# Kernel optimization log

Measured on AMD Instinct MI355X. Metric: run time of the kernel, lower is better.

## Reference

```python
import jax, jax.numpy as jnp
import numpy as np

B, N, D, H = 4, 1024, 1024, 16
NP = N - 1  # prototypes; +1 CLS slot -> n_valid == N
HD = D // H
LN_EPS = 1e-5


def _build_spatial_sim(key):
    centers = jax.random.uniform(key, (NP, 2), dtype=jnp.float32) * 10.0
    diff = centers[:, None, :] - centers[None, :, :]
    d2 = jnp.sum(diff * diff, axis=-1)           # squared pairwise distance
    dist = jnp.sqrt(d2)
    sigma = dist.mean()                           # spatial_sigma = mean cdist
    sim = jnp.exp(-d2 / (2.0 * sigma * sigma))
    sim = sim / sim.max()
    ext = jnp.zeros((NP + 1, NP + 1), dtype=jnp.float32)
    ext = ext.at[0, :].set(1.0).at[:, 0].set(1.0).at[1:, 1:].set(sim)
    return ext


def setup_inputs() -> dict:
    key = jax.random.key(0)
    kc, kx, kq, kp = jax.random.split(key, 4)
    spatial_sim = _build_spatial_sim(kc)          # [N, N] buffer
    x = jax.random.normal(kx, (B, N, D), dtype=jnp.float32)
    gamma = jnp.ones((D,), dtype=jnp.float32)
    beta = jnp.zeros((D,), dtype=jnp.float32)
    w_qkv = jax.random.normal(kq, (D, 3 * D), dtype=jnp.float32) * 0.02
    w_proj = jax.random.normal(kp, (D, D), dtype=jnp.float32) * 0.02
    b_proj = jnp.zeros((D,), dtype=jnp.float32)
    swl = jnp.float32(np.log(0.3 / 0.7))          # inverse_sigmoid(0.3)
    return {"x": x, "gamma": gamma, "beta": beta, "w_qkv": w_qkv,
            "w_proj": w_proj, "b_proj": b_proj,
            "spatial_weight_logit": swl, "spatial_sim": spatial_sim}


def reference(x, gamma, beta, w_qkv, w_proj, b_proj, spatial_weight_logit, spatial_sim):
    b, n, d = x.shape
    scale = HD ** (-0.5)
    # LayerNorm (biased variance, eps=1e-5)
    mu = x.mean(axis=-1, keepdims=True)
    var = jnp.mean((x - mu) ** 2, axis=-1, keepdims=True)
    x_norm = (x - mu) / jnp.sqrt(var + LN_EPS) * gamma + beta
    # QKV projection -> [B, H, N, HD] each
    qkv = (x_norm @ w_qkv).reshape(b, n, 3, H, HD)
    qkv = jnp.transpose(qkv, (2, 0, 3, 1, 4))
    q, k, v = qkv[0], qkv[1], qkv[2]
    scores = jnp.einsum('bhnd,bhmd->bhnm', q, k) * scale
    alpha = jax.nn.sigmoid(spatial_weight_logit)
    # blend feature attention with fixed spatial similarity, then softmax
    attn = jax.nn.softmax((1.0 - alpha) * scores + alpha * spatial_sim[None, None], axis=-1)
    out = jnp.einsum('bhnm,bhmd->bhnd', attn, v)
    out = jnp.transpose(out, (0, 2, 1, 3)).reshape(b, n, d)
    out = out @ w_proj + b_proj
    return x + out
```

## Files before the change

### kernel.cpp

```cpp
#include <hip/hip_runtime.h>

#define Bz 4
#define Nn 1024
#define Dd 1024
#define Hh 16
#define HD 64
#define SCALE 0.125f
#define LN_EPS 1e-5f

typedef __attribute__((ext_vector_type(8))) __bf16 bf16x8;
typedef __attribute__((ext_vector_type(4))) float f32x4;

static __device__ inline unsigned short f2bf(float f) {
    unsigned int u = __float_as_uint(f);
    u += 0x7fffu + ((u >> 16) & 1u);
    return (unsigned short)(u >> 16);
}

static __device__ inline bf16x8 ldfrag(const unsigned short* p) {
    return *(const bf16x8*)p;
}

static __device__ __forceinline__ void glds16(const unsigned short* g, unsigned short* l) {
    __builtin_amdgcn_global_load_lds((const __attribute__((address_space(1))) void*)g,
                                     (__attribute__((address_space(3))) void*)l, 16, 0, 0);
}

__global__ __launch_bounds__(256) void prep_kernel(const float* __restrict__ x,
                                                   const float* __restrict__ gamma,
                                                   const float* __restrict__ beta,
                                                   unsigned short* __restrict__ xn,
                                                   const float* __restrict__ w_qkv,
                                                   unsigned short* __restrict__ wqkvT,
                                                   const float* __restrict__ w_proj,
                                                   unsigned short* __restrict__ wprojT) {
    __shared__ float tile[32][33];
    int blk = blockIdx.x;
    int tid = threadIdx.x;

    if (blk < 4096) {
        const float* xr = x + (size_t)blk * Dd;
        float4 v = ((const float4*)xr)[tid];
        float s = v.x + v.y + v.z + v.w;
        float ss = v.x * v.x + v.y * v.y + v.z * v.z + v.w * v.w;
        for (int o = 32; o > 0; o >>= 1) {
            s += __shfl_down(s, o);
            ss += __shfl_down(ss, o);
        }
        float* red = &tile[0][0];
        int wid = tid >> 6;
        if ((tid & 63) == 0) { red[wid * 2] = s; red[wid * 2 + 1] = ss; }
        __syncthreads();
        float tot = red[0] + red[2] + red[4] + red[6];
        float tot2 = red[1] + red[3] + red[5] + red[7];
        float mu = tot * (1.0f / Dd);
        float var = tot2 * (1.0f / Dd) - mu * mu;
        float inv = rsqrtf(var + LN_EPS);
        float4 g = ((const float4*)gamma)[tid];
        float4 b = ((const float4*)beta)[tid];
        ushort4 o4;
        o4.x = f2bf((v.x - mu) * inv * g.x + b.x);
        o4.y = f2bf((v.y - mu) * inv * g.y + b.y);
        o4.z = f2bf((v.z - mu) * inv * g.z + b.z);
        o4.w = f2bf((v.w - mu) * inv * g.w + b.w);
        ((ushort4*)(xn + (size_t)blk * Dd))[tid] = o4;
    } else {
        const float* in;
        unsigned short* out;
        int cols, c0, r0;
        if (blk < 7168) {
            int idx = blk - 4096;
            in = w_qkv; out = wqkvT; cols = 3072;
            c0 = (idx % 96) * 32; r0 = (idx / 96) * 32;
        } else {
            int idx = blk - 7168;
            in = w_proj; out = wprojT; cols = 1024;
            c0 = (idx % 32) * 32; r0 = (idx / 32) * 32;
        }
        int tx = tid & 31, ty = tid >> 5;
        #pragma unroll
        for (int i = 0; i < 32; i += 8)
            tile[ty + i][tx] = in[(size_t)(r0 + ty + i) * cols + c0 + tx];
        __syncthreads();
        #pragma unroll
        for (int i = 0; i < 32; i += 8)
            out[(size_t)(c0 + ty + i) * 1024 + r0 + tx] = f2bf(tile[tx][ty + i]);
    }
}


__global__ __launch_bounds__(256) void gemm_qkv(const unsigned short* __restrict__ A,
                                                const unsigned short* __restrict__ Bt,
                                                unsigned short* __restrict__ qb,
                                                unsigned short* __restrict__ kb,
                                                unsigned short* __restrict__ vtb) {
    __shared__ unsigned short sA[8192], sB[8192];
    int tid = threadIdx.x;
    int w = tid >> 6, lane = tid & 63, lrow = lane & 15, quad = lane >> 4;
    int wm = w >> 1, wn = w & 1;
    int rowbase = blockIdx.y * 128;
    int colbase = blockIdx.x * 128;

    int srow = tid >> 3;
    int gch = ((tid & 7) - (srow >> 1)) & 7;
    const unsigned short* gA = A + (size_t)(rowbase + srow) * 1024 + gch * 8;
    const unsigned short* gB = Bt + (size_t)(colbase + srow) * 1024 + gch * 8;
    unsigned short* lA = sA + w * 512;
    unsigned short* lB = sB + w * 512;

    int bs0 = ((quad + (lrow >> 1)) & 7) * 8;
    int bs1 = ((4 + quad + (lrow >> 1)) & 7) * 8;
    const unsigned short* fa = sA + (wm * 64 + lrow) * 64;
    const unsigned short* fb = sB + (wn * 64 + lrow) * 64;

    f32x4 acc[4][4];
    #pragma unroll
    for (int i = 0; i < 4; i++)
        #pragma unroll
        for (int j = 0; j < 4; j++)
            acc[i][j] = (f32x4){0.f, 0.f, 0.f, 0.f};

    for (int k0 = 0; k0 < 1024; k0 += 64) {
        __syncthreads();
        #pragma unroll
        for (int c = 0; c < 4; c++) {
            glds16(gA + (size_t)c * 32768 + k0, lA + c * 2048);
            glds16(gB + (size_t)c * 32768 + k0, lB + c * 2048);
        }
        __syncthreads();
        #pragma unroll
        for (int s = 0; s < 2; s++) {
            int bo = s ? bs1 : bs0;
            bf16x8 a[4], b[4];
            #pragma unroll
            for (int i = 0; i < 4; i++) a[i] = *(const bf16x8*)(fa + i * 1024 + bo);
            #pragma unroll
            for (int j = 0; j < 4; j++) b[j] = *(const bf16x8*)(fb + j * 1024 + bo);
            #pragma unroll
            for (int i = 0; i < 4; i++)
                #pragma unroll
                for (int j = 0; j < 4; j++)
                    acc[i][j] = __builtin_amdgcn_mfma_f32_16x16x32_bf16(a[i], b[j], acc[i][j], 0, 0, 0);
        }
    }

    if (colbase < 2048) {
        #pragma unroll
        for (int j = 0; j < 4; j++) {
            int col = colbase + wn * 64 + j * 16 + lrow;
            int s = col >> 10, rem = col & 1023;
            int h = rem >> 6, e = rem & 63;
            unsigned short* dst = (s == 0) ? qb : kb;
            #pragma unroll
            for (int i = 0; i < 4; i++) {
                #pragma unroll
                for (int r = 0; r < 4; r++) {
                    int R = rowbase + wm * 64 + i * 16 + quad * 4 + r;
                    int bb = R >> 10, n = R & 1023;
                    dst[(((size_t)(bb * Hh + h)) * Nn + n) * HD + e] = f2bf(acc[i][j][r]);
                }
            }
        }
    } else {
        int bb = rowbase >> 10;
        int nbase = (rowbase & 1023) + wm * 64;
        unsigned short* sc = sA + w * 2048;
        int er = lane >> 2, nc = lane & 3;
        #pragma unroll
        for (int j = 0; j < 4; j++) {
            __syncthreads();
            int ebase = colbase + wn * 64 + j * 16 - 2048;
            int h = ebase >> 6, e0 = ebase & 63;
            #pragma unroll
            for (int i = 0; i < 4; i++) {
                uint2 pk;
                pk.x = (unsigned)f2bf(acc[i][j][0]) | ((unsigned)f2bf(acc[i][j][1]) << 16);
                pk.y = (unsigned)f2bf(acc[i][j][2]) | ((unsigned)f2bf(acc[i][j][3]) << 16);
                *(uint2*)(sc + lrow * 68 + i * 16 + quad * 4) = pk;
            }
            __syncthreads();
            unsigned short* vrow = vtb + ((size_t)((bb * Hh + h) * HD) + e0 + er) * Nn + nbase;
            #pragma unroll
            for (int c = 0; c < 4; c++) {
                uint2 v = *(const uint2*)(sc + er * 68 + c * 16 + nc * 4);
                *(uint2*)(vrow + c * 16 + nc * 4) = v;
            }
        }
    }
}

__global__ __launch_bounds__(256) void gemm_proj(const unsigned short* __restrict__ A,
                                                 const unsigned short* __restrict__ Bt,
                                                 const float* __restrict__ bias,
                                                 const float* __restrict__ x,
                                                 float* __restrict__ out) {
    __shared__ unsigned short sA[8192], sB[8192];
    int tid = threadIdx.x;
    int w = tid >> 6, lane = tid & 63, lrow = lane & 15, quad = lane >> 4;
    int wm = w >> 1, wn = w & 1;
    int rowbase = blockIdx.y * 128;
    int colbase = blockIdx.x * 128;

    int srow = tid >> 3;
    int gch = ((tid & 7) - (srow >> 1)) & 7;
    const unsigned short* gA = A + (size_t)(rowbase + srow) * 1024 + gch * 8;
    const unsigned short* gB = Bt + (size_t)(colbase + srow) * 1024 + gch * 8;
    unsigned short* lA = sA + w * 512;
    unsigned short* lB = sB + w * 512;

    int bs0 = ((quad + (lrow >> 1)) & 7) * 8;
    int bs1 = ((4 + quad + (lrow >> 1)) & 7) * 8;
    const unsigned short* fa = sA + (wm * 64 + lrow) * 64;
    const unsigned short* fb = sB + (wn * 64 + lrow) * 64;

    f32x4 acc[4][4];
    #pragma unroll
    for (int i = 0; i < 4; i++)
        #pragma unroll
        for (int j = 0; j < 4; j++)
            acc[i][j] = (f32x4){0.f, 0.f, 0.f, 0.f};

    for (int k0 = 0; k0 < 1024; k0 += 64) {
        __syncthreads();
        #pragma unroll
        for (int c = 0; c < 4; c++) {
            glds16(gA + (size_t)c * 32768 + k0, lA + c * 2048);
            glds16(gB + (size_t)c * 32768 + k0, lB + c * 2048);
        }
        __syncthreads();
        #pragma unroll
        for (int s = 0; s < 2; s++) {
            int bo = s ? bs1 : bs0;
            bf16x8 a[4], b[4];
            #pragma unroll
            for (int i = 0; i < 4; i++) a[i] = *(const bf16x8*)(fa + i * 1024 + bo);
            #pragma unroll
            for (int j = 0; j < 4; j++) b[j] = *(const bf16x8*)(fb + j * 1024 + bo);
            #pragma unroll
            for (int i = 0; i < 4; i++)
                #pragma unroll
                for (int j = 0; j < 4; j++)
                    acc[i][j] = __builtin_amdgcn_mfma_f32_16x16x32_bf16(a[i], b[j], acc[i][j], 0, 0, 0);
        }
    }

    #pragma unroll
    for (int j = 0; j < 4; j++) {
        int col = colbase + wn * 64 + j * 16 + lrow;
        float bc = bias[col];
        #pragma unroll
        for (int i = 0; i < 4; i++) {
            #pragma unroll
            for (int r = 0; r < 4; r++) {
                int R = rowbase + wm * 64 + i * 16 + quad * 4 + r;
                out[(size_t)R * 1024 + col] = acc[i][j][r] + bc + x[(size_t)R * 1024 + col];
            }
        }
    }
}

#define PSTR 72
__global__ __launch_bounds__(256) void attn_kernel(const unsigned short* __restrict__ qb,
                                                   const unsigned short* __restrict__ kb,
                                                   const unsigned short* __restrict__ vtb,
                                                   const float* __restrict__ sim,
                                                   const float* __restrict__ swl,
                                                   unsigned short* __restrict__ aout) {
    int h = blockIdx.y, bb = blockIdx.z;
    int n0 = blockIdx.x * 128;
    int tid = threadIdx.x;
    int w = tid >> 6, lane = tid & 63;
    int lrow = lane & 15, quad = lane >> 4;
    const unsigned short* q = qb + ((size_t)(bb * Hh + h)) * Nn * HD;
    const unsigned short* k = kb + ((size_t)(bb * Hh + h)) * Nn * HD;
    const unsigned short* vt = vtb + ((size_t)(bb * Hh + h)) * HD * Nn;
    float alpha = 1.f / (1.f + __expf(-swl[0]));
    float c1 = (1.f - alpha) * SCALE;

    __shared__ unsigned short sK[4096];
    __shared__ unsigned short sV[4096];
    __shared__ unsigned short sP[128 * PSTR];

    int qr0 = n0 + w * 32;
    bf16x8 qf[2][2];
    #pragma unroll
    for (int g = 0; g < 2; g++) {
        qf[g][0] = ldfrag(q + (size_t)(qr0 + g * 16 + lrow) * HD + quad * 8);
        qf[g][1] = ldfrag(q + (size_t)(qr0 + g * 16 + lrow) * HD + 32 + quad * 8);
    }

    f32x4 o[2][4];
    #pragma unroll
    for (int g = 0; g < 2; g++)
        #pragma unroll
        for (int et = 0; et < 4; et++) o[g][et] = (f32x4){0.f, 0.f, 0.f, 0.f};
    float rsum[2] = {0.f, 0.f};

    int bs0 = (quad + (lrow >> 1)) & 7;
    int bs1 = (4 + quad + (lrow >> 1)) & 7;
    unsigned short* sPw = sP + (w * 32) * PSTR;

    for (int m0 = 0; m0 < 1024; m0 += 64) {
        __syncthreads();
        #pragma unroll
        for (int i = 0; i < 2; i++) {
            int slot = i * 256 + tid;
            int row = slot >> 3;
            int cg = ((slot & 7) - (row >> 1)) & 7;
            glds16(k + (size_t)(m0 + row) * HD + cg * 8, sK + i * 2048 + w * 512);
        }
        #pragma unroll
        for (int i = 0; i < 2; i++) {
            int slot = i * 256 + tid;
            int row = slot >> 3;
            int cg = ((slot & 7) - (row >> 1)) & 7;
            glds16(vt + (size_t)row * Nn + m0 + cg * 8, sV + i * 2048 + w * 512);
        }
        float4 sm[4][2];
        #pragma unroll
        for (int ks = 0; ks < 4; ks++)
            #pragma unroll
            for (int g = 0; g < 2; g++)
                sm[ks][g] = *(const float4*)(sim + (size_t)(qr0 + g * 16 + lrow) * Nn
                                             + m0 + ks * 16 + quad * 4);
        __syncthreads();

        #pragma unroll
        for (int ks = 0; ks < 4; ks++) {
            const unsigned short* kr = sK + (ks * 16 + lrow) * 64;
            bf16x8 ak0 = *(const bf16x8*)(kr + bs0 * 8);
            bf16x8 ak1 = *(const bf16x8*)(kr + bs1 * 8);
            #pragma unroll
            for (int g = 0; g < 2; g++) {
                f32x4 c = (f32x4){0.f, 0.f, 0.f, 0.f};
                c = __builtin_amdgcn_mfma_f32_16x16x32_bf16(ak0, qf[g][0], c, 0, 0, 0);
                c = __builtin_amdgcn_mfma_f32_16x16x32_bf16(ak1, qf[g][1], c, 0, 0, 0);
                float e0 = __expf(c1 * c[0] + alpha * sm[ks][g].x);
                float e1 = __expf(c1 * c[1] + alpha * sm[ks][g].y);
                float e2 = __expf(c1 * c[2] + alpha * sm[ks][g].z);
                float e3 = __expf(c1 * c[3] + alpha * sm[ks][g].w);
                rsum[g] += (e0 + e1) + (e2 + e3);
                uint2 pk;
                pk.x = (__float_as_uint(e0) >> 16) | (__float_as_uint(e1) & 0xffff0000u);
                pk.y = (__float_as_uint(e2) >> 16) | (__float_as_uint(e3) & 0xffff0000u);
                *(uint2*)(sPw + (g * 16 + lrow) * PSTR + ks * 16 + quad * 4) = pk;
            }
        }

        #pragma unroll
        for (int ms = 0; ms < 2; ms++) {
            bf16x8 pa[2];
            #pragma unroll
            for (int g = 0; g < 2; g++)
                pa[g] = *(const bf16x8*)(sPw + (g * 16 + lrow) * PSTR + ms * 32 + quad * 8);
            #pragma unroll
            for (int et = 0; et < 4; et++) {
                int e = et * 16 + lrow;
                int slot = (ms * 4 + quad + (e >> 1)) & 7;
                bf16x8 vb = *(const bf16x8*)(sV + e * 64 + slot * 8);
                #pragma unroll
                for (int g = 0; g < 2; g++)
                    o[g][et] = __builtin_amdgcn_mfma_f32_16x16x32_bf16(pa[g], vb, o[g][et], 0, 0, 0);
            }
        }
    }

    #pragma unroll
    for (int g = 0; g < 2; g++) {
        rsum[g] += __shfl_xor(rsum[g], 16);
        rsum[g] += __shfl_xor(rsum[g], 32);
    }

    #pragma unroll
    for (int g = 0; g < 2; g++)
        #pragma unroll
        for (int r = 0; r < 4; r++) {
            float inv = 1.f / __shfl(rsum[g], quad * 4 + r);
            int qn = qr0 + g * 16 + quad * 4 + r;
            #pragma unroll
            for (int et = 0; et < 4; et++)
                aout[((size_t)bb * Nn + qn) * Dd + h * HD + et * 16 + lrow]
                    = f2bf(o[g][et][r] * inv);
        }
}

extern "C" void kernel_launch(void* const* d_in, const int* in_sizes, int n_in,
                              void* d_out, int out_size, void* d_ws, size_t ws_size,
                              hipStream_t stream) {
    const float* x      = (const float*)d_in[0];
    const float* gamma  = (const float*)d_in[1];
    const float* beta   = (const float*)d_in[2];
    const float* w_qkv  = (const float*)d_in[3];
    const float* w_proj = (const float*)d_in[4];
    const float* b_proj = (const float*)d_in[5];
    const float* swl    = (const float*)d_in[6];
    const float* sim    = (const float*)d_in[7];
    float* out = (float*)d_out;

    unsigned short* ws = (unsigned short*)d_ws;
    unsigned short* xn     = ws;
    unsigned short* wqkvT  = xn + 4194304;
    unsigned short* wprojT = wqkvT + 3145728;
    unsigned short* qb     = wprojT + 1048576;
    unsigned short* kb     = qb + 4194304;
    unsigned short* vtb    = kb + 4194304;
    unsigned short* aout   = vtb + 4194304;

    prep_kernel<<<8192, 256, 0, stream>>>(x, gamma, beta, xn, w_qkv, wqkvT, w_proj, wprojT);
    gemm_qkv<<<dim3(24, 32), 256, 0, stream>>>(xn, wqkvT, qb, kb, vtb);
    attn_kernel<<<dim3(8, 16, 4), 256, 0, stream>>>(qb, kb, vtb, sim, swl, aout);
    gemm_proj<<<dim3(8, 32), 256, 0, stream>>>(aout, wprojT, b_proj, x, out);
}
```

Before: 199.4 us.

## Fuse all stages into one cooperative persistent kernel with grid syncs

```diff
diff --git a/kernel.cpp b/kernel.cpp
--- a/kernel.cpp
+++ b/kernel.cpp
@@ -1,4 +1,7 @@
 #include <hip/hip_runtime.h>
+#include <hip/hip_cooperative_groups.h>
+
+namespace cg = cooperative_groups;
 
 #define Bz 4
 #define Nn 1024
@@ -26,80 +29,74 @@
                                      (__attribute__((address_space(3))) void*)l, 16, 0, 0);
 }
 
-__global__ __launch_bounds__(256) void prep_kernel(const float* __restrict__ x,
-                                                   const float* __restrict__ gamma,
-                                                   const float* __restrict__ beta,
-                                                   unsigned short* __restrict__ xn,
-                                                   const float* __restrict__ w_qkv,
-                                                   unsigned short* __restrict__ wqkvT,
-                                                   const float* __restrict__ w_proj,
-                                                   unsigned short* __restrict__ wprojT) {
-    __shared__ float tile[32][33];
-    int blk = blockIdx.x;
-    int tid = threadIdx.x;
-
-    if (blk < 4096) {
-        const float* xr = x + (size_t)blk * Dd;
-        float4 v = ((const float4*)xr)[tid];
-        float s = v.x + v.y + v.z + v.w;
-        float ss = v.x * v.x + v.y * v.y + v.z * v.z + v.w * v.w;
-        for (int o = 32; o > 0; o >>= 1) {
-            s += __shfl_down(s, o);
-            ss += __shfl_down(ss, o);
-        }
-        float* red = &tile[0][0];
-        int wid = tid >> 6;
-        if ((tid & 63) == 0) { red[wid * 2] = s; red[wid * 2 + 1] = ss; }
-        __syncthreads();
-        float tot = red[0] + red[2] + red[4] + red[6];
-        float tot2 = red[1] + red[3] + red[5] + red[7];
-        float mu = tot * (1.0f / Dd);
-        float var = tot2 * (1.0f / Dd) - mu * mu;
-        float inv = rsqrtf(var + LN_EPS);
-        float4 g = ((const float4*)gamma)[tid];
-        float4 b = ((const float4*)beta)[tid];
-        ushort4 o4;
-        o4.x = f2bf((v.x - mu) * inv * g.x + b.x);
-        o4.y = f2bf((v.y - mu) * inv * g.y + b.y);
-        o4.z = f2bf((v.z - mu) * inv * g.z + b.z);
-        o4.w = f2bf((v.w - mu) * inv * g.w + b.w);
-        ((ushort4*)(xn + (size_t)blk * Dd))[tid] = o4;
-    } else {
-        const float* in;
-        unsigned short* out;
-        int cols, c0, r0;
-        if (blk < 7168) {
-            int idx = blk - 4096;
-            in = w_qkv; out = wqkvT; cols = 3072;
-            c0 = (idx % 96) * 32; r0 = (idx / 96) * 32;
+static __device__ __forceinline__ void phase_prep(unsigned short* smem, int bid, int tid,
+        const float* __restrict__ x, const float* __restrict__ gamma,
+        const float* __restrict__ beta, unsigned short* __restrict__ xn,
+        const float* __restrict__ w_qkv, unsigned short* __restrict__ wqkvT,
+        const float* __restrict__ w_proj, unsigned short* __restrict__ wprojT) {
+    float* tile = (float*)smem;
+    for (int blk = bid; blk < 8192; blk += 512) {
+        if (blk < 4096) {
+            const float* xr = x + (size_t)blk * Dd;
+            float4 v = ((const float4*)xr)[tid];
+            float s = v.x + v.y + v.z + v.w;
+            float ss = v.x * v.x + v.y * v.y + v.z * v.z + v.w * v.w;
+            for (int o = 32; o > 0; o >>= 1) {
+                s += __shfl_down(s, o);
+                ss += __shfl_down(ss, o);
+            }
+            int wid = tid >> 6;
+            if ((tid & 63) == 0) { tile[wid * 2] = s; tile[wid * 2 + 1] = ss; }
+            __syncthreads();
+            float tot = tile[0] + tile[2] + tile[4] + tile[6];
+            float tot2 = tile[1] + tile[3] + tile[5] + tile[7];
+            float mu = tot * (1.0f / Dd);
+            float var = tot2 * (1.0f / Dd) - mu * mu;
+            float inv = rsqrtf(var + LN_EPS);
+            float4 g = ((const float4*)gamma)[tid];
+            float4 b = ((const float4*)beta)[tid];
+            ushort4 o4;
+            o4.x = f2bf((v.x - mu) * inv * g.x + b.x);
+            o4.y = f2bf((v.y - mu) * inv * g.y + b.y);
+            o4.z = f2bf((v.z - mu) * inv * g.z + b.z);
+            o4.w = f2bf((v.w - mu) * inv * g.w + b.w);
+            ((ushort4*)(xn + (size_t)blk * Dd))[tid] = o4;
         } else {
-            int idx = blk - 7168;
-            in = w_proj; out = wprojT; cols = 1024;
-            c0 = (idx % 32) * 32; r0 = (idx / 32) * 32;
-        }
-        int tx = tid & 31, ty = tid >> 5;
-        #pragma unroll
-        for (int i = 0; i < 32; i += 8)
-            tile[ty + i][tx] = in[(size_t)(r0 + ty + i) * cols + c0 + tx];
-        __syncthreads();
-        #pragma unroll
-        for (int i = 0; i < 32; i += 8)
-            out[(size_t)(c0 + ty + i) * 1024 + r0 + tx] = f2bf(tile[tx][ty + i]);
-    }
-}
-
-
-__global__ __launch_bounds__(256) void gemm_qkv(const unsigned short* __restrict__ A,
-                                                const unsigned short* __restrict__ Bt,
-                                                unsigned short* __restrict__ qb,
-                                                unsigned short* __restrict__ kb,
-                                                unsigned short* __restrict__ vtb) {
-    __shared__ unsigned short sA[8192], sB[8192];
-    int tid = threadIdx.x;
+            const float* in;
+            unsigned short* outp;
+            int cols, c0, r0;
+            if (blk < 7168) {
+                int idx = blk - 4096;
+                in = w_qkv; outp = wqkvT; cols = 3072;
+                c0 = (idx % 96) * 32; r0 = (idx / 96) * 32;
+            } else {
+                int idx = blk - 7168;
+                in = w_proj; outp = wprojT; cols = 1024;
+                c0 = (idx % 32) * 32; r0 = (idx / 32) * 32;
+            }
+            int tx = tid & 31, ty = tid >> 5;
+            #pragma unroll
+            for (int i = 0; i < 32; i += 8)
+                tile[(ty + i) * 33 + tx] = in[(size_t)(r0 + ty + i) * cols + c0 + tx];
+            __syncthreads();
+            #pragma unroll
+            for (int i = 0; i < 32; i += 8)
+                outp[(size_t)(c0 + ty + i) * 1024 + r0 + tx] = f2bf(tile[tx * 33 + ty + i]);
+        }
+        __syncthreads();
+    }
+}
+
+static __device__ __forceinline__ void phase_qkv(unsigned short* smem, int t, int tid,
+        const unsigned short* __restrict__ A, const unsigned short* __restrict__ Bt,
+        unsigned short* __restrict__ qb, unsigned short* __restrict__ kb,
+        unsigned short* __restrict__ vtb) {
+    unsigned short* sA = smem;
+    unsigned short* sB = smem + 8192;
     int w = tid >> 6, lane = tid & 63, lrow = lane & 15, quad = lane >> 4;
     int wm = w >> 1, wn = w & 1;
-    int rowbase = blockIdx.y * 128;
-    int colbase = blockIdx.x * 128;
+    int rowbase = (t >> 5) * 128;
+    int colbase = (t & 31) * 96;
 
     int srow = tid >> 3;
     int gch = ((tid & 7) - (srow >> 1)) & 7;
@@ -111,45 +108,47 @@
     int bs0 = ((quad + (lrow >> 1)) & 7) * 8;
     int bs1 = ((4 + quad + (lrow >> 1)) & 7) * 8;
     const unsigned short* fa = sA + (wm * 64 + lrow) * 64;
-    const unsigned short* fb = sB + (wn * 64 + lrow) * 64;
-
-    f32x4 acc[4][4];
+    const unsigned short* fb = sB + (wn * 48 + lrow) * 64;
+
+    f32x4 acc[4][3];
     #pragma unroll
     for (int i = 0; i < 4; i++)
         #pragma unroll
-        for (int j = 0; j < 4; j++)
+        for (int j = 0; j < 3; j++)
             acc[i][j] = (f32x4){0.f, 0.f, 0.f, 0.f};
 
     for (int k0 = 0; k0 < 1024; k0 += 64) {
         __syncthreads();
         #pragma unroll
-        for (int c = 0; c < 4; c++) {
+        for (int c = 0; c < 4; c++)
             glds16(gA + (size_t)c * 32768 + k0, lA + c * 2048);
+        #pragma unroll
+        for (int c = 0; c < 3; c++)
             glds16(gB + (size_t)c * 32768 + k0, lB + c * 2048);
-        }
         __syncthreads();
         #pragma unroll
         for (int s = 0; s < 2; s++) {
             int bo = s ? bs1 : bs0;
-            bf16x8 a[4], b[4];
+            bf16x8 a[4], b[3];
             #pragma unroll
             for (int i = 0; i < 4; i++) a[i] = *(const bf16x8*)(fa + i * 1024 + bo);
             #pragma unroll
-            for (int j = 0; j < 4; j++) b[j] = *(const bf16x8*)(fb + j * 1024 + bo);
+            for (int j = 0; j < 3; j++) b[j] = *(const bf16x8*)(fb + j * 1024 + bo);
             #pragma unroll
             for (int i = 0; i < 4; i++)
                 #pragma unroll
-                for (int j = 0; j < 4; j++)
+                for (int j = 0; j < 3; j++)
                     acc[i][j] = __builtin_amdgcn_mfma_f32_16x16x32_bf16(a[i], b[j], acc[i][j], 0, 0, 0);
         }
     }
 
-    if (colbase < 2048) {
-        #pragma unroll
-        for (int j = 0; j < 4; j++) {
-            int col = colbase + wn * 64 + j * 16 + lrow;
-            int s = col >> 10, rem = col & 1023;
-            int h = rem >> 6, e = rem & 63;
+    #pragma unroll
+    for (int j = 0; j < 3; j++) {
+        int colg = colbase + wn * 48 + j * 16;
+        int s = colg >> 10, rem = colg & 1023;
+        int h = rem >> 6;
+        int e = (rem & 63) + lrow;
+        if (s < 2) {
             unsigned short* dst = (s == 0) ? qb : kb;
             #pragma unroll
             for (int i = 0; i < 4; i++) {
@@ -160,126 +159,38 @@
                     dst[(((size_t)(bb * Hh + h)) * Nn + n) * HD + e] = f2bf(acc[i][j][r]);
                 }
             }
-        }
-    } else {
-        int bb = rowbase >> 10;
-        int nbase = (rowbase & 1023) + wm * 64;
-        unsigned short* sc = sA + w * 2048;
-        int er = lane >> 2, nc = lane & 3;
-        #pragma unroll
-        for (int j = 0; j < 4; j++) {
-            __syncthreads();
-            int ebase = colbase + wn * 64 + j * 16 - 2048;
-            int h = ebase >> 6, e0 = ebase & 63;
+        } else {
             #pragma unroll
             for (int i = 0; i < 4; i++) {
+                int R0 = rowbase + wm * 64 + i * 16 + quad * 4;
+                int bb = R0 >> 10, n0v = R0 & 1023;
                 uint2 pk;
                 pk.x = (unsigned)f2bf(acc[i][j][0]) | ((unsigned)f2bf(acc[i][j][1]) << 16);
                 pk.y = (unsigned)f2bf(acc[i][j][2]) | ((unsigned)f2bf(acc[i][j][3]) << 16);
-                *(uint2*)(sc + lrow * 68 + i * 16 + quad * 4) = pk;
-            }
-            __syncthreads();
-            unsigned short* vrow = vtb + ((size_t)((bb * Hh + h) * HD) + e0 + er) * Nn + nbase;
-            #pragma unroll
-            for (int c = 0; c < 4; c++) {
-                uint2 v = *(const uint2*)(sc + er * 68 + c * 16 + nc * 4);
-                *(uint2*)(vrow + c * 16 + nc * 4) = v;
-            }
-        }
-    }
-}
-
-__global__ __launch_bounds__(256) void gemm_proj(const unsigned short* __restrict__ A,
-                                                 const unsigned short* __restrict__ Bt,
-                                                 const float* __restrict__ bias,
-                                                 const float* __restrict__ x,
-                                                 float* __restrict__ out) {
-    __shared__ unsigned short sA[8192], sB[8192];
-    int tid = threadIdx.x;
+                *(uint2*)(vtb + ((size_t)((bb * Hh + h) * HD) + e) * Nn + n0v) = pk;
+            }
+        }
+    }
+}
+
+static __device__ __forceinline__ void phase_attn(unsigned short* smem, int bid, int tid,
+        const unsigned short* __restrict__ qb, const unsigned short* __restrict__ kb,
+        const unsigned short* __restrict__ vtb, const float* __restrict__ sim,
+        const float* __restrict__ swl, unsigned short* __restrict__ aout) {
+    int nt = bid & 7, h = (bid >> 3) & 15, bb = bid >> 7;
+    int n0 = nt * 128;
     int w = tid >> 6, lane = tid & 63, lrow = lane & 15, quad = lane >> 4;
-    int wm = w >> 1, wn = w & 1;
-    int rowbase = blockIdx.y * 128;
-    int colbase = blockIdx.x * 128;
-
-    int srow = tid >> 3;
-    int gch = ((tid & 7) - (srow >> 1)) & 7;
-    const unsigned short* gA = A + (size_t)(rowbase + srow) * 1024 + gch * 8;
-    const unsigned short* gB = Bt + (size_t)(colbase + srow) * 1024 + gch * 8;
-    unsigned short* lA = sA + w * 512;
-    unsigned short* lB = sB + w * 512;
-
-    int bs0 = ((quad + (lrow >> 1)) & 7) * 8;
-    int bs1 = ((4 + quad + (lrow >> 1)) & 7) * 8;
-    const unsigned short* fa = sA + (wm * 64 + lrow) * 64;
-    const unsigned short* fb = sB + (wn * 64 + lrow) * 64;
-
-    f32x4 acc[4][4];
-    #pragma unroll
-    for (int i = 0; i < 4; i++)
-        #pragma unroll
-        for (int j = 0; j < 4; j++)
-            acc[i][j] = (f32x4){0.f, 0.f, 0.f, 0.f};
-
-    for (int k0 = 0; k0 < 1024; k0 += 64) {
-        __syncthreads();
-        #pragma unroll
-        for (int c = 0; c < 4; c++) {
-            glds16(gA + (size_t)c * 32768 + k0, lA + c * 2048);
-            glds16(gB + (size_t)c * 32768 + k0, lB + c * 2048);
-        }
-        __syncthreads();
-        #pragma unroll
-        for (int s = 0; s < 2; s++) {
-            int bo = s ? bs1 : bs0;
-            bf16x8 a[4], b[4];
-            #pragma unroll
-            for (int i = 0; i < 4; i++) a[i] = *(const bf16x8*)(fa + i * 1024 + bo);
-            #pragma unroll
-            for (int j = 0; j < 4; j++) b[j] = *(const bf16x8*)(fb + j * 1024 + bo);
-            #pragma unroll
-            for (int i = 0; i < 4; i++)
-                #pragma unroll
-                for (int j = 0; j < 4; j++)
-                    acc[i][j] = __builtin_amdgcn_mfma_f32_16x16x32_bf16(a[i], b[j], acc[i][j], 0, 0, 0);
-        }
-    }
-
-    #pragma unroll
-    for (int j = 0; j < 4; j++) {
-        int col = colbase + wn * 64 + j * 16 + lrow;
-        float bc = bias[col];
-        #pragma unroll
-        for (int i = 0; i < 4; i++) {
-            #pragma unroll
-            for (int r = 0; r < 4; r++) {
-                int R = rowbase + wm * 64 + i * 16 + quad * 4 + r;
-                out[(size_t)R * 1024 + col] = acc[i][j][r] + bc + x[(size_t)R * 1024 + col];
-            }
-        }
-    }
-}
-
-#define PSTR 72
-__global__ __launch_bounds__(256) void attn_kernel(const unsigned short* __restrict__ qb,
-                                                   const unsigned short* __restrict__ kb,
-                                                   const unsigned short* __restrict__ vtb,
-                                                   const float* __restrict__ sim,
-                                                   const float* __restrict__ swl,
-                                                   unsigned short* __restrict__ aout) {
-    int h = blockIdx.y, bb = blockIdx.z;
-    int n0 = blockIdx.x * 128;
-    int tid = threadIdx.x;
-    int w = tid >> 6, lane = tid & 63;
-    int lrow = lane & 15, quad = lane >> 4;
     const unsigned short* q = qb + ((size_t)(bb * Hh + h)) * Nn * HD;
     const unsigned short* k = kb + ((size_t)(bb * Hh + h)) * Nn * HD;
     const unsigned short* vt = vtb + ((size_t)(bb * Hh + h)) * HD * Nn;
     float alpha = 1.f / (1.f + __expf(-swl[0]));
-    float c1 = (1.f - alpha) * SCALE;
-
-    __shared__ unsigned short sK[4096];
-    __shared__ unsigned short sV[4096];
-    __shared__ unsigned short sP[128 * PSTR];
+    const float L2E = 1.44269504f;
+    float c1 = (1.f - alpha) * SCALE * L2E;
+    float aL = alpha * L2E;
+
+    unsigned short* sK = smem;
+    unsigned short* sV = smem + 4096;
+    unsigned short* sP = smem + 8192;
 
     int qr0 = n0 + w * 32;
     bf16x8 qf[2][2];
@@ -298,7 +209,9 @@
 
     int bs0 = (quad + (lrow >> 1)) & 7;
     int bs1 = (4 + quad + (lrow >> 1)) & 7;
-    unsigned short* sPw = sP + (w * 32) * PSTR;
+    unsigned short* sPw = sP + (w * 32) * 64;
+    int psw = lrow & 7;
+    int wrc = quad >> 1, wrh = quad & 1;
 
     for (int m0 = 0; m0 < 1024; m0 += 64) {
         __syncthreads();
@@ -306,15 +219,15 @@
         for (int i = 0; i < 2; i++) {
             int slot = i * 256 + tid;
             int row = slot >> 3;
-            int cg = ((slot & 7) - (row >> 1)) & 7;
-            glds16(k + (size_t)(m0 + row) * HD + cg * 8, sK + i * 2048 + w * 512);
+            int cg2 = ((slot & 7) - (row >> 1)) & 7;
+            glds16(k + (size_t)(m0 + row) * HD + cg2 * 8, sK + i * 2048 + w * 512);
         }
         #pragma unroll
         for (int i = 0; i < 2; i++) {
             int slot = i * 256 + tid;
             int row = slot >> 3;
-            int cg = ((slot & 7) - (row >> 1)) & 7;
-            glds16(vt + (size_t)row * Nn + m0 + cg * 8, sV + i * 2048 + w * 512);
+            int cg2 = ((slot & 7) - (row >> 1)) & 7;
+            glds16(vt + (size_t)row * Nn + m0 + cg2 * 8, sV + i * 2048 + w * 512);
         }
         float4 sm[4][2];
         #pragma unroll
@@ -330,20 +243,21 @@
             const unsigned short* kr = sK + (ks * 16 + lrow) * 64;
             bf16x8 ak0 = *(const bf16x8*)(kr + bs0 * 8);
             bf16x8 ak1 = *(const bf16x8*)(kr + bs1 * 8);
+            int cc = ((ks * 2 + wrc) ^ psw);
             #pragma unroll
             for (int g = 0; g < 2; g++) {
                 f32x4 c = (f32x4){0.f, 0.f, 0.f, 0.f};
                 c = __builtin_amdgcn_mfma_f32_16x16x32_bf16(ak0, qf[g][0], c, 0, 0, 0);
                 c = __builtin_amdgcn_mfma_f32_16x16x32_bf16(ak1, qf[g][1], c, 0, 0, 0);
-                float e0 = __expf(c1 * c[0] + alpha * sm[ks][g].x);
-                float e1 = __expf(c1 * c[1] + alpha * sm[ks][g].y);
-                float e2 = __expf(c1 * c[2] + alpha * sm[ks][g].z);
-                float e3 = __expf(c1 * c[3] + alpha * sm[ks][g].w);
+                float e0 = exp2f(c1 * c[0] + aL * sm[ks][g].x);
+                float e1 = exp2f(c1 * c[1] + aL * sm[ks][g].y);
+                float e2 = exp2f(c1 * c[2] + aL * sm[ks][g].z);
+                float e3 = exp2f(c1 * c[3] + aL * sm[ks][g].w);
                 rsum[g] += (e0 + e1) + (e2 + e3);
                 uint2 pk;
                 pk.x = (__float_as_uint(e0) >> 16) | (__float_as_uint(e1) & 0xffff0000u);
                 pk.y = (__float_as_uint(e2) >> 16) | (__float_as_uint(e3) & 0xffff0000u);
-                *(uint2*)(sPw + (g * 16 + lrow) * PSTR + ks * 16 + quad * 4) = pk;
+                *(uint2*)(sPw + (g * 16 + lrow) * 64 + cc * 8 + wrh * 4) = pk;
             }
         }
 
@@ -352,7 +266,8 @@
             bf16x8 pa[2];
             #pragma unroll
             for (int g = 0; g < 2; g++)
-                pa[g] = *(const bf16x8*)(sPw + (g * 16 + lrow) * PSTR + ms * 32 + quad * 8);
+                pa[g] = *(const bf16x8*)(sPw + (g * 16 + lrow) * 64
+                                         + ((ms * 4 + quad) ^ psw) * 8);
             #pragma unroll
             for (int et = 0; et < 4; et++) {
                 int e = et * 16 + lrow;
@@ -382,6 +297,121 @@
                 aout[((size_t)bb * Nn + qn) * Dd + h * HD + et * 16 + lrow]
                     = f2bf(o[g][et][r] * inv);
         }
+}
+
+static __device__ __forceinline__ void phase_proj(unsigned short* smem, int bid, int tid,
+        const unsigned short* __restrict__ A, const unsigned short* __restrict__ Bt,
+        const float* __restrict__ bias, const float* __restrict__ x,
+        float* __restrict__ out) {
+    unsigned short* sA = smem;
+    unsigned short* sB = smem + 4096;
+    int w = tid >> 6, lane = tid & 63, lrow = lane & 15, quad = lane >> 4;
+    int wm = w >> 1, wn = w & 1;
+    int rowbase = (bid >> 3) * 64;
+    int colbase = (bid & 7) * 128;
+
+    int srow = tid >> 3;
+    int gch = ((tid & 7) - (srow >> 1)) & 7;
+    const unsigned short* gA = A + (size_t)(rowbase + srow) * 1024 + gch * 8;
+    const unsigned short* gB = Bt + (size_t)(colbase + srow) * 1024 + gch * 8;
+    unsigned short* lA = sA + w * 512;
+    unsigned short* lB = sB + w * 512;
+
+    int bs0 = ((quad + (lrow >> 1)) & 7) * 8;
+    int bs1 = ((4 + quad + (lrow >> 1)) & 7) * 8;
+    const unsigned short* fa = sA + (wm * 32 + lrow) * 64;
+    const unsigned short* fb = sB + (wn * 64 + lrow) * 64;
+
+    f32x4 acc[2][4];
+    #pragma unroll
+    for (int i = 0; i < 2; i++)
+        #pragma unroll
+        for (int j = 0; j < 4; j++)
+            acc[i][j] = (f32x4){0.f, 0.f, 0.f, 0.f};
+
+    for (int k0 = 0; k0 < 1024; k0 += 64) {
+        __syncthreads();
+        #pragma unroll
+        for (int c = 0; c < 2; c++)
+            glds16(gA + (size_t)c * 32768 + k0, lA + c * 2048);
+        #pragma unroll
+        for (int c = 0; c < 4; c++)
+            glds16(gB + (size_t)c * 32768 + k0, lB + c * 2048);
+        __syncthreads();
+        #pragma unroll
+        for (int s = 0; s < 2; s++) {
+            int bo = s ? bs1 : bs0;
+            bf16x8 a[2], b[4];
+            #pragma unroll
+            for (int i = 0; i < 2; i++) a[i] = *(const bf16x8*)(fa + i * 1024 + bo);
+            #pragma unroll
+            for (int j = 0; j < 4; j++) b[j] = *(const bf16x8*)(fb + j * 1024 + bo);
+            #pragma unroll
+            for (int i = 0; i < 2; i++)
+                #pragma unroll
+                for (int j = 0; j < 4; j++)
+                    acc[i][j] = __builtin_amdgcn_mfma_f32_16x16x32_bf16(a[i], b[j], acc[i][j], 0, 0, 0);
+        }
+    }
+
+    #pragma unroll
+    for (int j = 0; j < 4; j++) {
+        int col = colbase + wn * 64 + j * 16 + lrow;
+        float bc = bias[col];
+        #pragma unroll
+        for (int i = 0; i < 2; i++) {
+            #pragma unroll
+            for (int r = 0; r < 4; r++) {
+                int R = rowbase + wm * 32 + i * 16 + quad * 4 + r;
+                out[(size_t)R * 1024 + col] = acc[i][j][r] + bc + x[(size_t)R * 1024 + col];
+            }
+        }
+    }
+}
+
+__global__ __launch_bounds__(256, 2) void mega(const float* x, const float* gamma,
+        const float* beta, const float* w_qkv, const float* w_proj,
+        const float* b_proj, const float* swl, const float* sim, float* out,
+        unsigned short* xn, unsigned short* wqkvT, unsigned short* wprojT,
+        unsigned short* qb, unsigned short* kb, unsigned short* vtb,
+        unsigned short* aout) {
+    cg::grid_group grid = cg::this_grid();
+    __shared__ __align__(16) unsigned short smem[16384];
+    int tid = threadIdx.x, bid = blockIdx.x;
+
+    phase_prep(smem, bid, tid, x, gamma, beta, xn, w_qkv, wqkvT, w_proj, wprojT);
+    grid.sync();
+    phase_qkv(smem, bid, tid, xn, wqkvT, qb, kb, vtb);
+    phase_qkv(smem, bid + 512, tid, xn, wqkvT, qb, kb, vtb);
+    grid.sync();
+    phase_attn(smem, bid, tid, qb, kb, vtb, sim, swl, aout);
+    grid.sync();
+    phase_proj(smem, bid, tid, aout, wprojT, b_proj, x, out);
+}
+
+__global__ __launch_bounds__(256) void k_prep(const float* x, const float* gamma,
+        const float* beta, unsigned short* xn, const float* w_qkv,
+        unsigned short* wqkvT, const float* w_proj, unsigned short* wprojT) {
+    __shared__ __align__(16) unsigned short smem[16384];
+    phase_prep(smem, blockIdx.x, threadIdx.x, x, gamma, beta, xn, w_qkv, wqkvT, w_proj, wprojT);
+}
+__global__ __launch_bounds__(256) void k_qkv(const unsigned short* A,
+        const unsigned short* Bt, unsigned short* qb, unsigned short* kb,
+        unsigned short* vtb) {
+    __shared__ __align__(16) unsigned short smem[16384];
+    phase_qkv(smem, blockIdx.x, threadIdx.x, A, Bt, qb, kb, vtb);
+    phase_qkv(smem, blockIdx.x + 512, threadIdx.x, A, Bt, qb, kb, vtb);
+}
+__global__ __launch_bounds__(256) void k_attn(const unsigned short* qb,
+        const unsigned short* kb, const unsigned short* vtb, const float* sim,
+        const float* swl, unsigned short* aout) {
+    __shared__ __align__(16) unsigned short smem[16384];
+    phase_attn(smem, blockIdx.x, threadIdx.x, qb, kb, vtb, sim, swl, aout);
+}
+__global__ __launch_bounds__(256) void k_proj(const unsigned short* A,
+        const unsigned short* Bt, const float* bias, const float* x, float* out) {
+    __shared__ __align__(16) unsigned short smem[16384];
+    phase_proj(smem, blockIdx.x, threadIdx.x, A, Bt, bias, x, out);
 }
 
 extern "C" void kernel_launch(void* const* d_in, const int* in_sizes, int n_in,
@@ -406,8 +436,19 @@
     unsigned short* vtb    = kb + 4194304;
     unsigned short* aout   = vtb + 4194304;
 
-    prep_kernel<<<8192, 256, 0, stream>>>(x, gamma, beta, xn, w_qkv, wqkvT, w_proj, wprojT);
-    gemm_qkv<<<dim3(24, 32), 256, 0, stream>>>(xn, wqkvT, qb, kb, vtb);
-    attn_kernel<<<dim3(8, 16, 4), 256, 0, stream>>>(qb, kb, vtb, sim, swl, aout);
-    gemm_proj<<<dim3(8, 32), 256, 0, stream>>>(aout, wprojT, b_proj, x, out);
-}
+    void* args[] = {
+        (void*)&x, (void*)&gamma, (void*)&beta, (void*)&w_qkv, (void*)&w_proj,
+        (void*)&b_proj, (void*)&swl, (void*)&sim, (void*)&out,
+        (void*)&xn, (void*)&wqkvT, (void*)&wprojT,
+        (void*)&qb, (void*)&kb, (void*)&vtb, (void*)&aout
+    };
+    hipError_t err = hipLaunchCooperativeKernel((const void*)mega, dim3(512), dim3(256),
+                                                args, 0, stream);
+    if (err != hipSuccess) {
+        (void)hipGetLastError();
+        k_prep<<<512, 256, 0, stream>>>(x, gamma, beta, xn, w_qkv, wqkvT, w_proj, wprojT);
+        k_qkv<<<512, 256, 0, stream>>>(xn, wqkvT, qb, kb, vtb);
+        k_attn<<<512, 256, 0, stream>>>(qb, kb, vtb, sim, swl, aout);
+        k_proj<<<512, 256, 0, stream>>>(aout, wprojT, b_proj, x, out);
+    }
+}
```

Result: slower. 396.2 us (+98.6%).
